# Kernel optimization log

Measured on AMD Instinct MI355X. Metric: run time of the kernel, lower is better.

The kernel has to match this reference:

```python
import jax, jax.numpy as jnp
import numpy as np

B, S, D, H = 2, 2048, 1024, 16
DK = D // H


def setup_inputs() -> dict:
    key = jax.random.key(0)
    ks = jax.random.split(key, 9)
    w_scale = 1.0 / np.sqrt(D)  # xavier-ish scale
    return {
        "q": jax.random.normal(ks[0], (B, S, D), dtype=jnp.float32),
        "k": jax.random.normal(ks[1], (B, S, D), dtype=jnp.float32),
        "v": jax.random.normal(ks[2], (B, S, D), dtype=jnp.float32),
        "A": jax.random.uniform(ks[3], (S, S), dtype=jnp.float32),
        "Wq": jax.random.normal(ks[4], (D, D), dtype=jnp.float32) * w_scale,
        "bq": jnp.zeros((D,), jnp.float32),
        "Wk": jax.random.normal(ks[5], (D, D), dtype=jnp.float32) * w_scale,
        "bk": jnp.zeros((D,), jnp.float32),
        "Wv": jax.random.normal(ks[6], (D, D), dtype=jnp.float32) * w_scale,
        "bv": jnp.zeros((D,), jnp.float32),
        "Wo": jax.random.normal(ks[7], (D, D), dtype=jnp.float32) * w_scale,
        "bo": jnp.zeros((D,), jnp.float32),
    }


def _proj(x, W, b):
    # nn.Linear: x @ W^T + b, then split heads -> [B, H, S, DK]
    y = jnp.einsum("bsd,ed->bse", x, W) + b
    return y.reshape(B, S, H, DK).transpose(0, 2, 1, 3)


def reference(q, k, v, A, Wq, bq, Wk, bk, Wv, bv, Wo, bo):
    qh = _proj(q, Wq, bq)  # [B,H,S,DK]
    kh = _proj(k, Wk, bk)
    vh = _proj(v, Wv, bv)
    scale = 1.0 / jnp.sqrt(jnp.asarray(DK, qh.dtype))
    scores = jnp.einsum("bhqd,bhkd->bhqk", qh, kh) * scale  # [B,H,S,S]
    # No softmax: scores multiplied by structural mask A^T (dropout disabled, eval)
    p_attn = scores * A.T
    x = jnp.einsum("bhqk,bhkd->bhqd", p_attn, vh)
    x = x.transpose(0, 2, 1, 3).reshape(B, S, D)
    return jnp.einsum("bsd,ed->bse", x, Wo) + bo
```

## Files before the change

### kernel.cpp

```cpp
#include <hip/hip_runtime.h>

#define SEQ    2048
#define DMODEL 1024
#define NHEAD  16
#define DHEAD  64
#define NBATCH 2

typedef __bf16 bf16x8 __attribute__((ext_vector_type(8)));
typedef float f32x16 __attribute__((ext_vector_type(16)));
typedef float f32x8 __attribute__((ext_vector_type(8)));
typedef unsigned short ushort8v __attribute__((ext_vector_type(8)));
typedef unsigned int uint2v __attribute__((ext_vector_type(2)));
typedef int int4v __attribute__((ext_vector_type(4)));

static __device__ __forceinline__ unsigned short f2b(float f){
  unsigned int u = __builtin_bit_cast(unsigned int, f);
  u += 0x7fffu + ((u>>16)&1u);
  return (unsigned short)(u>>16);
}
static __device__ __forceinline__ float b2f(unsigned short h){
  unsigned int u = ((unsigned int)h)<<16;
  return __builtin_bit_cast(float, u);
}
static __device__ __forceinline__ f32x16 mfma32(bf16x8 a, bf16x8 b, f32x16 c){
  return __builtin_amdgcn_mfma_f32_32x32x16_bf16(a,b,c,0,0,0);
}
static __device__ __forceinline__ ushort8v cvt8(const float* p){
  float4 f0 = *(const float4*)p;
  float4 f1 = *(const float4*)(p+4);
  ushort8v r;
  r[0]=f2b(f0.x); r[1]=f2b(f0.y); r[2]=f2b(f0.z); r[3]=f2b(f0.w);
  r[4]=f2b(f1.x); r[5]=f2b(f1.y); r[6]=f2b(f1.z); r[7]=f2b(f1.w);
  return r;
}
#define GLOAD16(g,l) __builtin_amdgcn_global_load_lds( \
    (const __attribute__((address_space(1))) void*)(g), \
    (__attribute__((address_space(3))) void*)(l), 16, 0, 0)

__global__ __launch_bounds__(256) void cvtXpack(
    const float* __restrict__ q, const float* __restrict__ k, const float* __restrict__ v,
    unsigned short* __restrict__ Xq, unsigned short* __restrict__ Xk, unsigned short* __restrict__ Xv)
{
  const int z = blockIdx.z;
  const float* S = (z==0)? q : (z==1)? k : v;
  unsigned short* D = (z==0)? Xq : (z==1)? Xk : Xv;
  const int g = blockIdx.x;
  const int wave = threadIdx.x>>6, lane = threadIdx.x&63;
  const int l31 = lane&31, hi = lane>>5;
  const float* src = S + (size_t)(g*32 + l31)*DMODEL + 8*hi + 256*wave;
  unsigned short* dst = D + (size_t)(g*64 + wave*16)*512 + lane*8;
  #pragma unroll
  for (int i=0;i<16;i++)
    *(ushort8v*)(dst + (size_t)i*512) = cvt8(src + 16*i);
}

__global__ __launch_bounds__(256) void cvtWpack(
    const float* __restrict__ Wq, const float* __restrict__ Wk,
    const float* __restrict__ Wv, const float* __restrict__ Wo,
    unsigned short* __restrict__ Wp)
{
  const int z = blockIdx.z;
  const float* S = (z==0)? Wq : (z==1)? Wk : (z==2)? Wv : Wo;
  const int g = blockIdx.x;
  const int wave = threadIdx.x>>6, lane = threadIdx.x&63;
  const int l31 = lane&31, hi = lane>>5;
  const float* src = S + (size_t)(g*32 + l31)*DMODEL + 8*hi + 256*wave;
  unsigned short* dst = Wp + (size_t)((z*32 + g)*64 + wave*16)*512 + lane*8;
  #pragma unroll
  for (int i=0;i<16;i++)
    *(ushort8v*)(dst + (size_t)i*512) = cvt8(src + 16*i);
}

__global__ __launch_bounds__(256) void cvtA(const float* __restrict__ A,
                                            unsigned short* __restrict__ Am){
  const int tid  = threadIdx.x;
  const int lane = tid&63, l31 = lane&31, hi = lane>>5;
  const int q32  = blockIdx.x;
  const int kt   = blockIdx.y*4 + (tid>>6);
  const int q    = q32*32 + l31;

  unsigned short out8[4][8];
  #pragma unroll
  for (int fi=0; fi<2; fi++){
    #pragma unroll
    for (int mm=0; mm<4; mm++){
      #pragma unroll
      for (int j=0; j<4; j++){
        const int k = kt*64 + 32*fi + 8*mm + 4*hi + j;
        out8[fi*2 + (mm>>1)][(mm&1)*4 + j] = f2b(A[(size_t)k*SEQ + q]);
      }
    }
  }
  unsigned short* dst = Am + ((size_t)(q32*32 + kt)*4)*512 + lane*8;
  #pragma unroll
  for (int w=0; w<4; w++)
    *(ushort8v*)(dst + (size_t)w*512) = *(const ushort8v*)out8[w];
}

__global__ __launch_bounds__(256,3) void proj_qkv(
    const unsigned short* __restrict__ Xq, const unsigned short* __restrict__ Xk, const unsigned short* __restrict__ Xv,
    const unsigned short* __restrict__ Wp,
    const float* __restrict__ bq, const float* __restrict__ bk, const float* __restrict__ bv,
    unsigned short* __restrict__ qh, unsigned short* __restrict__ Kp, unsigned short* __restrict__ Vp)
{
  const int z = blockIdx.z;
  const unsigned short* X = (z==0)? Xq : (z==1)? Xk : Xv;
  const unsigned short* W = Wp + (size_t)z*1048576;
  const float* bias = (z==0)? bq : (z==1)? bk : bv;
  const float alpha = (z==0)? 0.125f : 1.0f;

  const int orig = blockIdx.y*8 + blockIdx.x;
  const int virt = (orig&7)*32 + (orig>>3);
  const int bx = virt&7, by = virt>>3;
  const int mb = by*128, nb = bx*128;

  const int tid = threadIdx.x;
  const int lane = tid&63, wave = tid>>6;
  const int wr = wave>>1, wc = wave&1, l31 = lane&31, hi = lane>>5;
  f32x16 acc[2][2] = {};

  const unsigned short* a0p = X + (size_t)((mb>>5) + 2*wr)*32768 + lane*8;
  const unsigned short* a1p = a0p + 32768;
  const unsigned short* b0p = W + (size_t)((nb>>5) + 2*wc)*32768 + lane*8;
  const unsigned short* b1p = b0p + 32768;

  #pragma unroll 4
  for (int s=0;s<64;s++){
    bf16x8 a0 = *(const bf16x8*)(a0p + (size_t)s*512);
    bf16x8 a1 = *(const bf16x8*)(a1p + (size_t)s*512);
    bf16x8 b0 = *(const bf16x8*)(b0p + (size_t)s*512);
    bf16x8 b1 = *(const bf16x8*)(b1p + (size_t)s*512);
    acc[0][0] = mfma32(a0,b0,acc[0][0]);
    acc[0][1] = mfma32(a0,b1,acc[0][1]);
    acc[1][0] = mfma32(a1,b0,acc[1][0]);
    acc[1][1] = mfma32(a1,b1,acc[1][1]);
  }

  #pragma unroll
  for (int fj=0; fj<2; fj++){
    const int e = nb + 64*wc + 32*fj + l31;
    const float bv_ = bias[e];
    const int hh = e>>6, dk = e&63;
    #pragma unroll
    for (int fi=0; fi<2; fi++){
      #pragma unroll
      for (int r=0;r<16;r++){
        const int i = mb + 64*wr + 32*fi + (r&3) + 8*(r>>2) + 4*hi;
        const int bb = i>>11, ss = i&(SEQ-1);
        const int bhh = bb*NHEAD + hh;
        const unsigned short val = f2b((acc[fi][fj][r] + bv_)*alpha);
        if (z==0){
          qh[((size_t)bhh*SEQ + ss)*DHEAD + dk] = val;
        } else if (z==1){
          const size_t addr = (((size_t)(bhh*64 + (ss>>5))*4 + (dk>>4))*64
                               + ((dk>>3)&1)*32 + (ss&31))*8 + (dk&7);
          Kp[addr] = val;
        } else {
          const size_t addr = ((((size_t)(bhh*32 + (ss>>6))*4 + ((ss>>4)&3))*2
                               + (dk>>5))*64 + ((ss>>3)&1)*32 + (dk&31))*8 + (ss&7);
          Vp[addr] = val;
        }
      }
    }
  }
}

__global__ __launch_bounds__(512,4) void attn(
    const unsigned short* __restrict__ qh, const unsigned short* __restrict__ Kp,
    const unsigned short* __restrict__ Vp, const unsigned short* __restrict__ Am,
    unsigned short* __restrict__ xp)
{
  const int orig = blockIdx.y*16 + blockIdx.x;
  const int xcd = orig&7, within = orig>>3;
  const int bh   = xcd*4 + (within>>4);
  const int qblk = within&15;

  const int tid  = threadIdx.x;
  const int lane = tid&63, wave = tid>>6;
  const int qsub = wave&3, khalf = wave>>2;
  const int l31 = lane&31, hi = lane>>5;

  const int q32  = qblk*4 + qsub;
  const int qrow = q32*32 + l31;
  const unsigned short* qp = qh + ((size_t)bh*SEQ + qrow)*DHEAD;
  bf16x8 Qf[4];
  #pragma unroll
  for (int t=0;t<4;t++) Qf[t] = *(const bf16x8*)(qp + 16*t + 8*hi);

  f32x16 xacc[2] = {};

  const unsigned short* kpb = Kp + (size_t)bh*131072 + lane*8;
  const unsigned short* vpb = Vp + (size_t)bh*131072 + lane*8;
  const unsigned short* apb = Am + (size_t)q32*65536 + lane*8;

  __shared__ float SMEMf[8448];
  unsigned short* smem = (unsigned short*)SMEMf;

  const unsigned short* gsb = ((wave<4)? kpb : vpb);
  const int fo = (wave&3)*2;
  const int dof = ((wave<4)? 0 : 4096) + fo*512;

  ushort8v Aa[2], Ab[2];

  #define STAGE(BUF, KT) { \
    const unsigned short* _g = gsb + (size_t)(KT)*4096 + (size_t)fo*512; \
    GLOAD16(_g,       smem + (BUF)*8192 + dof); \
    GLOAD16(_g + 512, smem + (BUF)*8192 + dof + 512); }

  #define LOADA(DST, KT) { \
    const unsigned short* _ap = apb + (size_t)(KT)*2048 + (size_t)(khalf*2)*512; \
    DST[0] = *(const ushort8v*)(_ap); \
    DST[1] = *(const ushort8v*)(_ap + 512); }

  STAGE(0, 0);
  LOADA(Aa, 0);
  __syncthreads();

  #define BODY(KT, BUF, AR, AN) { \
    STAGE((BUF)^1, ((KT)+1)&31); \
    LOADA(AN, ((KT)+1)&31); \
    unsigned int wv[4], xv[4]; \
    { \
      f32x16 sacc = {}; \
      _Pragma("unroll") \
      for (int s=0;s<4;s++){ \
        bf16x8 kf = *(const bf16x8*)(smem + (BUF)*8192 + (khalf*4+s)*512 + lane*8); \
        sacc = mfma32(kf, Qf[s], sacc); \
      } \
      ushort8v a80 = AR[0], a81 = AR[1]; \
      _Pragma("unroll") \
      for (int mm=0; mm<4; mm++){ \
        const int b0 = (mm&1)*4, rb2 = 4*mm; \
        float p0 = sacc[rb2+0]*((mm>>1)? b2f(a81[b0+0]) : b2f(a80[b0+0])); \
        float p1 = sacc[rb2+1]*((mm>>1)? b2f(a81[b0+1]) : b2f(a80[b0+1])); \
        float p2 = sacc[rb2+2]*((mm>>1)? b2f(a81[b0+2]) : b2f(a80[b0+2])); \
        float p3 = sacc[rb2+3]*((mm>>1)? b2f(a81[b0+3]) : b2f(a80[b0+3])); \
        asm("v_cvt_pk_bf16_f32 %0, %1, %2" : "=v"(wv[mm]) : "v"(p0), "v"(p1)); \
        asm("v_cvt_pk_bf16_f32 %0, %1, %2" : "=v"(xv[mm]) : "v"(p2), "v"(p3)); \
      } \
    } \
    __builtin_amdgcn_s_setprio(1); \
    _Pragma("unroll") \
    for (int sl=0; sl<2; sl++){ \
      const int s2 = 2*khalf + sl; \
      uint2v rw = __builtin_amdgcn_permlane32_swap(wv[2*sl], wv[2*sl+1], false, false); \
      uint2v rx = __builtin_amdgcn_permlane32_swap(xv[2*sl], xv[2*sl+1], false, false); \
      int4v av; av.x = (int)rw[0]; av.y = (int)rx[0]; av.z = (int)rw[1]; av.w = (int)rx[1]; \
      bf16x8 pa = __builtin_bit_cast(bf16x8, av); \
      bf16x8 v0 = *(const bf16x8*)(smem + (BUF)*8192 + 4096 + (s2*2+0)*512 + lane*8); \
      bf16x8 v1 = *(const bf16x8*)(smem + (BUF)*8192 + 4096 + (s2*2+1)*512 + lane*8); \
      xacc[0] = mfma32(pa, v0, xacc[0]); \
      xacc[1] = mfma32(pa, v1, xacc[1]); \
    } \
    __builtin_amdgcn_s_setprio(0); \
    __syncthreads(); }

  #pragma unroll 1
  for (int tt=0; tt<16; tt++){
    BODY(2*tt,   0, Aa, Ab);
    BODY(2*tt+1, 1, Ab, Aa);
  }
  #undef BODY
  #undef STAGE
  #undef LOADA

  float* red = SMEMf;
  if (khalf==1){
    #pragma unroll
    for (int j=0;j<2;j++)
      #pragma unroll
      for (int r=0;r<16;r++)
        red[((qsub*64 + lane)*33) + 16*j + r] = xacc[j][r];
  }
  __syncthreads();
  if (khalf==0){
    #pragma unroll
    for (int j=0;j<2;j++)
      #pragma unroll
      for (int r=0;r<16;r++)
        xacc[j][r] += red[((qsub*64 + lane)*33) + 16*j + r];
    const int b = bh>>4, h = bh&15;
    #pragma unroll
    for (int fj=0; fj<2; fj++){
      const int scol = h*4 + fj*2 + (l31>>4);
      const int lpart = ((l31>>3)&1)*32;
      const int epart = l31&7;
      #pragma unroll
      for (int r=0;r<16;r++){
        const int qq = q32*32 + (r&3) + 8*(r>>2) + 4*hi;
        const int row = b*SEQ + qq;
        const size_t addr = ((size_t)(row>>5)*64 + scol)*512 + (lpart + (row&31))*8 + epart;
        xp[addr] = f2b(xacc[fj][r]);
      }
    }
  }
}

__global__ __launch_bounds__(256,4) void oproj(
    const unsigned short* __restrict__ Xp, const unsigned short* __restrict__ Wop,
    const float* __restrict__ bo, float* __restrict__ out)
{
  const int orig = blockIdx.y*16 + blockIdx.x;
  const int virt = (orig&7)*64 + (orig>>3);
  const int bx = virt&15, by = virt>>4;
  const int mb = by*128, nb = bx*64;

  const int tid = threadIdx.x;
  const int lane = tid&63, wave = tid>>6;
  const int l31 = lane&31, hi = lane>>5;
  f32x16 acc[2] = {};

  const unsigned short* ap  = Xp  + (size_t)((mb>>5) + wave)*32768 + lane*8;
  const unsigned short* b0p = Wop + (size_t)(nb>>5)*32768 + lane*8;
  const unsigned short* b1p = b0p + 32768;

  #pragma unroll 4
  for (int s=0;s<64;s++){
    bf16x8 a  = *(const bf16x8*)(ap  + (size_t)s*512);
    bf16x8 b0 = *(const bf16x8*)(b0p + (size_t)s*512);
    bf16x8 b1 = *(const bf16x8*)(b1p + (size_t)s*512);
    acc[0] = mfma32(a,b0,acc[0]);
    acc[1] = mfma32(a,b1,acc[1]);
  }

  #pragma unroll
  for (int fj=0; fj<2; fj++){
    const int e = nb + 32*fj + l31;
    const float bv_ = bo[e];
    #pragma unroll
    for (int r=0;r<16;r++){
      const int i = mb + 32*wave + (r&3) + 8*(r>>2) + 4*hi;
      out[(size_t)i*DMODEL + e] = acc[fj][r] + bv_;
    }
  }
}

extern "C" void kernel_launch(void* const* d_in, const int* in_sizes, int n_in,
                              void* d_out, int out_size, void* d_ws, size_t ws_size,
                              hipStream_t stream)
{
  const float* q  = (const float*)d_in[0];
  const float* k  = (const float*)d_in[1];
  const float* v  = (const float*)d_in[2];
  const float* A  = (const float*)d_in[3];
  const float* Wq = (const float*)d_in[4];
  const float* bq = (const float*)d_in[5];
  const float* Wk = (const float*)d_in[6];
  const float* bk = (const float*)d_in[7];
  const float* Wv = (const float*)d_in[8];
  const float* bv = (const float*)d_in[9];
  const float* Wo = (const float*)d_in[10];
  const float* bo = (const float*)d_in[11];
  float* out = (float*)d_out;

  unsigned short* ws = (unsigned short*)d_ws;
  const size_t NE = (size_t)NBATCH*SEQ*DMODEL;
  unsigned short* qh  = ws;
  unsigned short* Kp  = qh + NE;
  unsigned short* Vp  = Kp + NE;
  unsigned short* xb  = Vp + NE;
  unsigned short* Wp  = xb + NE;
  unsigned short* Xqp = (unsigned short*)d_out;
  unsigned short* Xkp = Xqp + NE;
  unsigned short* Am  = (unsigned short*)d_out;
  unsigned short* Xvp = xb;

  cvtXpack<<<dim3(128, 1, 3), 256, 0, stream>>>(q, k, v, Xqp, Xkp, Xvp);
  cvtWpack<<<dim3(32, 1, 4), 256, 0, stream>>>(Wq, Wk, Wv, Wo, Wp);
  proj_qkv<<<dim3(8, 32, 3), 256, 0, stream>>>(
      Xqp, Xkp, Xvp, Wp, bq, bk, bv, qh, Kp, Vp);
  cvtA<<<dim3(64, 8), 256, 0, stream>>>(A, Am);
  attn<<<dim3(16, 32), 512, 0, stream>>>(qh, Kp, Vp, Am, xb);
  oproj<<<dim3(16, 32), 256, 0, stream>>>(xb, Wp + (size_t)3*1048576, bo, out);
}
```

Baseline: 133.5 us.

## Merge X/W conversion kernels and stage two KV tiles per barrier in attention

The X and W fp32-to-bf16 pack kernels are merged into one launch, with the fourth z-slice handling the four weight matrices. This removes one kernel launch. The attention loop now stages two K/V tiles and their A-mask fragments per pipeline step, so there is one __syncthreads per pair of tiles instead of one per tile. In exchange, LDS use roughly doubles to 64KB per block and register pressure rises from the extra A-fragment buffers, which may lower occupancy.

New measurement: 130.7 us. 2.1% less time.

```diff
diff --git a/kernel.cpp b/kernel.cpp
--- a/kernel.cpp
+++ b/kernel.cpp
@@ -37,35 +37,31 @@
     (const __attribute__((address_space(1))) void*)(g), \
     (__attribute__((address_space(3))) void*)(l), 16, 0, 0)
 
-__global__ __launch_bounds__(256) void cvtXpack(
+__global__ __launch_bounds__(256) void cvtXW(
     const float* __restrict__ q, const float* __restrict__ k, const float* __restrict__ v,
-    unsigned short* __restrict__ Xq, unsigned short* __restrict__ Xk, unsigned short* __restrict__ Xv)
+    const float* __restrict__ Wq, const float* __restrict__ Wk,
+    const float* __restrict__ Wv, const float* __restrict__ Wo,
+    unsigned short* __restrict__ Xq, unsigned short* __restrict__ Xk, unsigned short* __restrict__ Xv,
+    unsigned short* __restrict__ Wp)
 {
   const int z = blockIdx.z;
-  const float* S = (z==0)? q : (z==1)? k : v;
-  unsigned short* D = (z==0)? Xq : (z==1)? Xk : Xv;
-  const int g = blockIdx.x;
   const int wave = threadIdx.x>>6, lane = threadIdx.x&63;
   const int l31 = lane&31, hi = lane>>5;
+  const float* S;
+  unsigned short* dst;
+  int g;
+  if (z < 3){
+    S = (z==0)? q : (z==1)? k : v;
+    unsigned short* D = (z==0)? Xq : (z==1)? Xk : Xv;
+    g = blockIdx.x;
+    dst = D + (size_t)(g*64 + wave*16)*512 + lane*8;
+  } else {
+    const int wz = blockIdx.x>>5, gg = blockIdx.x&31;
+    S = (wz==0)? Wq : (wz==1)? Wk : (wz==2)? Wv : Wo;
+    g = gg;
+    dst = Wp + (size_t)((wz*32 + gg)*64 + wave*16)*512 + lane*8;
+  }
   const float* src = S + (size_t)(g*32 + l31)*DMODEL + 8*hi + 256*wave;
-  unsigned short* dst = D + (size_t)(g*64 + wave*16)*512 + lane*8;
-  #pragma unroll
-  for (int i=0;i<16;i++)
-    *(ushort8v*)(dst + (size_t)i*512) = cvt8(src + 16*i);
-}
-
-__global__ __launch_bounds__(256) void cvtWpack(
-    const float* __restrict__ Wq, const float* __restrict__ Wk,
-    const float* __restrict__ Wv, const float* __restrict__ Wo,
-    unsigned short* __restrict__ Wp)
-{
-  const int z = blockIdx.z;
-  const float* S = (z==0)? Wq : (z==1)? Wk : (z==2)? Wv : Wo;
-  const int g = blockIdx.x;
-  const int wave = threadIdx.x>>6, lane = threadIdx.x&63;
-  const int l31 = lane&31, hi = lane>>5;
-  const float* src = S + (size_t)(g*32 + l31)*DMODEL + 8*hi + 256*wave;
-  unsigned short* dst = Wp + (size_t)((z*32 + g)*64 + wave*16)*512 + lane*8;
   #pragma unroll
   for (int i=0;i<16;i++)
     *(ushort8v*)(dst + (size_t)i*512) = cvt8(src + 16*i);
@@ -193,38 +189,40 @@
   const unsigned short* vpb = Vp + (size_t)bh*131072 + lane*8;
   const unsigned short* apb = Am + (size_t)q32*65536 + lane*8;
 
-  __shared__ float SMEMf[8448];
+  __shared__ float SMEMf[16384];
   unsigned short* smem = (unsigned short*)SMEMf;
 
   const unsigned short* gsb = ((wave<4)? kpb : vpb);
   const int fo = (wave&3)*2;
   const int dof = ((wave<4)? 0 : 4096) + fo*512;
 
-  ushort8v Aa[2], Ab[2];
-
-  #define STAGE(BUF, KT) { \
-    const unsigned short* _g = gsb + (size_t)(KT)*4096 + (size_t)fo*512; \
-    GLOAD16(_g,       smem + (BUF)*8192 + dof); \
-    GLOAD16(_g + 512, smem + (BUF)*8192 + dof + 512); }
-
-  #define LOADA(DST, KT) { \
-    const unsigned short* _ap = apb + (size_t)(KT)*2048 + (size_t)(khalf*2)*512; \
-    DST[0] = *(const ushort8v*)(_ap); \
-    DST[1] = *(const ushort8v*)(_ap + 512); }
-
-  STAGE(0, 0);
-  LOADA(Aa, 0);
+  ushort8v Aa[2][2], Ab[2][2];
+
+  #define STAGE2(BUF, PT) { \
+    _Pragma("unroll") \
+    for (int tp=0; tp<2; tp++){ \
+      const unsigned short* _g = gsb + (size_t)((PT)*2+tp)*4096 + (size_t)fo*512; \
+      GLOAD16(_g,       smem + (BUF)*16384 + tp*8192 + dof); \
+      GLOAD16(_g + 512, smem + (BUF)*16384 + tp*8192 + dof + 512); } }
+
+  #define LOADA2(DST, PT) { \
+    _Pragma("unroll") \
+    for (int tp=0; tp<2; tp++){ \
+      const unsigned short* _ap = apb + (size_t)((PT)*2+tp)*2048 + (size_t)(khalf*2)*512; \
+      DST[tp][0] = *(const ushort8v*)(_ap); \
+      DST[tp][1] = *(const ushort8v*)(_ap + 512); } }
+
+  STAGE2(0, 0);
+  LOADA2(Aa, 0);
   __syncthreads();
 
-  #define BODY(KT, BUF, AR, AN) { \
-    STAGE((BUF)^1, ((KT)+1)&31); \
-    LOADA(AN, ((KT)+1)&31); \
+  #define TILE(BUF, TP, AR) { \
     unsigned int wv[4], xv[4]; \
     { \
       f32x16 sacc = {}; \
       _Pragma("unroll") \
       for (int s=0;s<4;s++){ \
-        bf16x8 kf = *(const bf16x8*)(smem + (BUF)*8192 + (khalf*4+s)*512 + lane*8); \
+        bf16x8 kf = *(const bf16x8*)(smem + (BUF)*16384 + (TP)*8192 + (khalf*4+s)*512 + lane*8); \
         sacc = mfma32(kf, Qf[s], sacc); \
       } \
       ushort8v a80 = AR[0], a81 = AR[1]; \
@@ -247,22 +245,29 @@
       uint2v rx = __builtin_amdgcn_permlane32_swap(xv[2*sl], xv[2*sl+1], false, false); \
       int4v av; av.x = (int)rw[0]; av.y = (int)rx[0]; av.z = (int)rw[1]; av.w = (int)rx[1]; \
       bf16x8 pa = __builtin_bit_cast(bf16x8, av); \
-      bf16x8 v0 = *(const bf16x8*)(smem + (BUF)*8192 + 4096 + (s2*2+0)*512 + lane*8); \
-      bf16x8 v1 = *(const bf16x8*)(smem + (BUF)*8192 + 4096 + (s2*2+1)*512 + lane*8); \
+      bf16x8 v0 = *(const bf16x8*)(smem + (BUF)*16384 + (TP)*8192 + 4096 + (s2*2+0)*512 + lane*8); \
+      bf16x8 v1 = *(const bf16x8*)(smem + (BUF)*16384 + (TP)*8192 + 4096 + (s2*2+1)*512 + lane*8); \
       xacc[0] = mfma32(pa, v0, xacc[0]); \
       xacc[1] = mfma32(pa, v1, xacc[1]); \
     } \
-    __builtin_amdgcn_s_setprio(0); \
+    __builtin_amdgcn_s_setprio(0); }
+
+  #define BODYP(BUF, PT, AR, AN) { \
+    STAGE2((BUF)^1, ((PT)+1)&15); \
+    LOADA2(AN, ((PT)+1)&15); \
+    TILE(BUF, 0, AR[0]); \
+    TILE(BUF, 1, AR[1]); \
     __syncthreads(); }
 
   #pragma unroll 1
-  for (int tt=0; tt<16; tt++){
-    BODY(2*tt,   0, Aa, Ab);
-    BODY(2*tt+1, 1, Ab, Aa);
-  }
-  #undef BODY
-  #undef STAGE
-  #undef LOADA
+  for (int uu=0; uu<8; uu++){
+    BODYP(0, 2*uu,   Aa, Ab);
+    BODYP(1, 2*uu+1, Ab, Aa);
+  }
+  #undef BODYP
+  #undef TILE
+  #undef STAGE2
+  #undef LOADA2
 
   float* red = SMEMf;
   if (khalf==1){
@@ -365,8 +370,8 @@
   unsigned short* Am  = (unsigned short*)d_out;
   unsigned short* Xvp = xb;
 
-  cvtXpack<<<dim3(128, 1, 3), 256, 0, stream>>>(q, k, v, Xqp, Xkp, Xvp);
-  cvtWpack<<<dim3(32, 1, 4), 256, 0, stream>>>(Wq, Wk, Wv, Wo, Wp);
+  cvtXW<<<dim3(128, 1, 4), 256, 0, stream>>>(q, k, v, Wq, Wk, Wv, Wo,
+                                             Xqp, Xkp, Xvp, Wp);
   proj_qkv<<<dim3(8, 32, 3), 256, 0, stream>>>(
       Xqp, Xkp, Xvp, Wp, bq, bk, bv, qh, Kp, Vp);
   cvtA<<<dim3(64, 8), 256, 0, stream>>>(A, Am);
```
